# Kernel tuning notes

Hardware: AMD Instinct MI355X
Metric: run time of the kernel (lower is better)

The kernel has to match this reference:

```python
import jax, jax.numpy as jnp
import numpy as np

N, E = 100000, 1600000
DIN, DH, DOUT = 128, 64, 4


def setup_inputs() -> dict:
    key = jax.random.key(0)
    ks = jax.random.split(key, 16)
    dims = [(DIN, DH), (DH, DH), (DH, DH), (DH, DH), (DH, DH), (DH, DOUT)]
    inp = {
        "x": jax.random.normal(ks[0], (N, DIN), dtype=jnp.float32),
        "edge_index": jax.random.randint(ks[1], (2, E), 0, N, dtype=jnp.int32),
    }
    for i, (di, do) in enumerate(dims):
        scale = 1.0 / np.sqrt(di)
        inp[f"W{i}"] = jax.random.normal(ks[2 + i], (di, do), dtype=jnp.float32) * scale
        inp[f"b{i}"] = jnp.zeros((do,), dtype=jnp.float32)
    return inp


def _gcn_graph(edge_index, n):
    # PyG gcn_norm with self-loops: D^{-1/2} (A+I) D^{-1/2}
    loops = jnp.arange(n, dtype=edge_index.dtype)
    src = jnp.concatenate([edge_index[0], loops])  # message sources
    dst = jnp.concatenate([edge_index[1], loops])  # aggregation targets
    deg = jax.ops.segment_sum(jnp.ones(src.shape[0], jnp.float32), dst, num_segments=n)
    dinv = jnp.where(deg > 0, jax.lax.rsqrt(deg), 0.0)
    norm = dinv[src] * dinv[dst]  # [E+N]
    return src, dst, norm


def _gcn_layer(x, src, dst, norm, W, b, n):
    h = x @ W                                   # [N, dout] dense transform first (PyG order)
    msg = h[src] * norm[:, None]                # gather + scale, [E+N, dout]
    return jax.ops.segment_sum(msg, dst, num_segments=n) + b


def reference(x, edge_index, W0, b0, W1, b1, W2, b2, W3, b3, W4, b4, W5, b5):
    n = x.shape[0]
    src, dst, norm = _gcn_graph(edge_index, n)
    Ws = [W0, W1, W2, W3, W4, W5]
    bs = [b0, b1, b2, b3, b4, b5]
    for i in range(len(Ws)):
        x = _gcn_layer(x, src, dst, norm, Ws[i], bs[i], n)
        if i < len(Ws) - 1:
            # eval mode: dropout / edge_dropout are identity
            x = jnp.where(x >= 0, x, 0.2 * x)  # leaky_relu, negative_slope=0.2
    return x
```

## Files before the change

kernel.cpp:

```cpp
#include <hip/hip_runtime.h>


__device__ __forceinline__ float readlane_f(float v, int l) {
    union { float f; int i; } u;
    u.f = v;
    u.i = __builtin_amdgcn_readlane(u.i, l);
    return u.f;
}

__global__ __launch_bounds__(256) void bucket_hist(const int* __restrict__ dst,
                                                   int* __restrict__ ghist,
                                                   int E, int NB) {
    __shared__ int h[1024];
    for (int i = threadIdx.x; i < NB; i += 256) h[i] = 0;
    __syncthreads();
    int i = blockIdx.x * blockDim.x + threadIdx.x;
    int stride = gridDim.x * blockDim.x;
    for (; i < E; i += stride) atomicAdd(&h[dst[i] >> 7], 1);
    __syncthreads();
    for (int j = threadIdx.x; j < NB; j += 256) {
        int c = h[j];
        if (c) atomicAdd(&ghist[j], c);
    }
}

__global__ void bucket_scan(const int* __restrict__ ghist, int* __restrict__ base,
                            int* __restrict__ cursor, int NB, int E) {
    int tid = threadIdx.x, lane = tid & 63, wid = tid >> 6;
    int v = (tid < NB) ? ghist[tid] : 0;
    int incl = v;
#pragma unroll
    for (int off = 1; off < 64; off <<= 1) {
        int t = __shfl_up(incl, off);
        if (lane >= off) incl += t;
    }
    __shared__ int ws[16];
    if (lane == 63) ws[wid] = incl;
    __syncthreads();
    if (tid == 0) {
        int run = 0;
        for (int i = 0; i < 16; ++i) { int t = ws[i]; ws[i] = run; run += t; }
    }
    __syncthreads();
    int excl = ws[wid] + incl - v;
    if (tid < NB) { base[tid] = excl; cursor[tid] = excl; }
    if (tid == 0) base[NB] = E;
}

__global__ __launch_bounds__(256) void bucket_scatter(
    const int* __restrict__ src, const int* __restrict__ dst,
    int* __restrict__ cursor, int* __restrict__ bsrc,
    unsigned char* __restrict__ bdl, int E, int NB) {
    __shared__ int h[1024];
    __shared__ int rb[1024];
    const int CH = 4096;
    for (int c0 = blockIdx.x * CH; c0 < E; c0 += gridDim.x * CH) {
        int cend = c0 + CH < E ? c0 + CH : E;
        for (int j = threadIdx.x; j < NB; j += 256) h[j] = 0;
        __syncthreads();
        for (int i = c0 + threadIdx.x; i < cend; i += 256)
            atomicAdd(&h[dst[i] >> 7], 1);
        __syncthreads();
        for (int j = threadIdx.x; j < NB; j += 256) {
            int c = h[j];
            rb[j] = c ? atomicAdd(&cursor[j], c) : 0;
            h[j] = 0;
        }
        __syncthreads();
        for (int i = c0 + threadIdx.x; i < cend; i += 256) {
            int d = dst[i];
            int b = d >> 7;
            int p = rb[b] + atomicAdd(&h[b], 1);
            bsrc[p] = src[i];
            bdl[p] = (unsigned char)(d & 127);
        }
        __syncthreads();
    }
}

__global__ __launch_bounds__(256) void bucket_finalize(
    const int* __restrict__ base, const int* __restrict__ bsrc,
    const unsigned char* __restrict__ bdl, int* __restrict__ rowptr,
    int* __restrict__ ssrc, float* __restrict__ dinv, int N, int NB, int E) {
    __shared__ int cnt[128];
    __shared__ int cur[128];
    __shared__ int w0sum;
    const int tid = threadIdx.x;
    const int lane = tid & 63;
    for (int b = blockIdx.x; b < NB; b += gridDim.x) {
        const int s = base[b], e = base[b + 1];
        const int d0 = b << 7;
        const int w = (N - d0 < 128) ? (N - d0) : 128;
        if (tid < 128) cnt[tid] = 0;
        __syncthreads();
        for (int i = s + tid; i < e; i += 256) atomicAdd(&cnt[bdl[i]], 1);
        __syncthreads();
        int v = (tid < 128) ? cnt[tid] : 0;
        int incl = v;
#pragma unroll
        for (int off = 1; off < 64; off <<= 1) {
            int t = __shfl_up(incl, off);
            if (lane >= off) incl += t;
        }
        if (tid == 63) w0sum = incl;
        __syncthreads();
        int excl = incl - v + ((tid >= 64 && tid < 128) ? w0sum : 0);
        if (tid < 128) cur[tid] = s + excl;
        if (tid < w) {
            rowptr[d0 + tid] = s + excl;
            dinv[d0 + tid] = rsqrtf((float)(v + 1));
        }
        __syncthreads();
        for (int i = s + tid; i < e; i += 256) {
            int p = atomicAdd(&cur[bdl[i]], 1);
            ssrc[p] = bsrc[i];
        }
        __syncthreads();
    }
    if (blockIdx.x == 0 && tid == 0) rowptr[N] = E;
}

template <int K, bool LRELU>
__global__ __launch_bounds__(256) void gemm_hs(
    const float* __restrict__ in, const float* __restrict__ W,
    const float* __restrict__ dinv, float* __restrict__ hs, int n) {
    const int lane = threadIdx.x & 63;
    const int gw = blockIdx.x * (blockDim.x >> 6) + (threadIdx.x >> 6);
    const int nw = gridDim.x * (blockDim.x >> 6);

    float wreg[K];
#pragma unroll
    for (int k = 0; k < K; ++k) wreg[k] = W[k * 64 + lane];

    for (int row = gw; row < n; row += nw) {
        float xv0 = in[(size_t)row * K + lane];
        if (LRELU) xv0 = xv0 >= 0.f ? xv0 : 0.2f * xv0;
        float xv1 = 0.f;
        if (K == 128) xv1 = in[(size_t)row * K + 64 + lane];
        float a0 = 0.f, a1 = 0.f, a2 = 0.f, a3 = 0.f;
#pragma unroll
        for (int k = 0; k < 64; k += 4) {
            a0 = fmaf(readlane_f(xv0, k + 0), wreg[k + 0], a0);
            a1 = fmaf(readlane_f(xv0, k + 1), wreg[k + 1], a1);
            a2 = fmaf(readlane_f(xv0, k + 2), wreg[k + 2], a2);
            a3 = fmaf(readlane_f(xv0, k + 3), wreg[k + 3], a3);
        }
        if (K == 128) {
#pragma unroll
            for (int k = 0; k < 64; k += 4) {
                a0 = fmaf(readlane_f(xv1, k + 0), wreg[64 + k + 0], a0);
                a1 = fmaf(readlane_f(xv1, k + 1), wreg[64 + k + 1], a1);
                a2 = fmaf(readlane_f(xv1, k + 2), wreg[64 + k + 2], a2);
                a3 = fmaf(readlane_f(xv1, k + 3), wreg[64 + k + 3], a3);
            }
        }
        float acc = (a0 + a1) + (a2 + a3);
        hs[(size_t)row * 64 + lane] = dinv[row] * acc;
    }
}

__global__ __launch_bounds__(256) void csr_agg_stream(
    const float* __restrict__ hs, const int* __restrict__ rowptr,
    const int* __restrict__ ssrc, const float* __restrict__ dinv,
    const float* __restrict__ b, float* __restrict__ y,
    int N, int E, int nwaves) {
    const int lane = threadIdx.x & 63;
    const int w = blockIdx.x * (blockDim.x >> 6) + (threadIdx.x >> 6);
    if (w >= nwaves) return;
    const float bl = b[lane];

    auto lb = [&](long long t) {
        int lo = 0, hi = N;
        while (lo < hi) {
            int m = (lo + hi) >> 1;
            if ((long long)rowptr[m] < t) lo = m + 1; else hi = m;
        }
        return lo;
    };
    const long long q0 = (long long)w * E / nwaves;
    const long long q1 = (long long)(w + 1) * E / nwaves;
    int r0 = lb(q0);
    int r1 = (w == nwaves - 1) ? N : lb(q1);

    for (int d = r0; d < r1; ++d) {
        int e = __builtin_amdgcn_readfirstlane(rowptr[d]);
        const int end = __builtin_amdgcn_readfirstlane(rowptr[d + 1]);
        float acc0 = hs[(size_t)d * 64 + lane];
        float acc1 = 0.f;
        for (; e + 8 <= end; e += 8) {
            int s0 = ssrc[e + 0], s1 = ssrc[e + 1];
            int s2 = ssrc[e + 2], s3 = ssrc[e + 3];
            int s4 = ssrc[e + 4], s5 = ssrc[e + 5];
            int s6 = ssrc[e + 6], s7 = ssrc[e + 7];
            float v0 = hs[(size_t)s0 * 64 + lane];
            float v1 = hs[(size_t)s1 * 64 + lane];
            float v2 = hs[(size_t)s2 * 64 + lane];
            float v3 = hs[(size_t)s3 * 64 + lane];
            float v4 = hs[(size_t)s4 * 64 + lane];
            float v5 = hs[(size_t)s5 * 64 + lane];
            float v6 = hs[(size_t)s6 * 64 + lane];
            float v7 = hs[(size_t)s7 * 64 + lane];
            acc0 += v0 + v2;
            acc1 += v1 + v3;
            acc0 += v4 + v6;
            acc1 += v5 + v7;
        }
        for (; e < end; ++e) {
            int s = ssrc[e];
            acc0 += hs[(size_t)s * 64 + lane];
        }
        y[(size_t)d * 64 + lane] = fmaf(dinv[d], acc0 + acc1, bl);
    }
}

__global__ __launch_bounds__(256) void gemm4_hs(
    const float* __restrict__ y, const float* __restrict__ W,
    const float* __restrict__ dinv, float* __restrict__ hs4, int n) {
    int i = blockIdx.x * blockDim.x + threadIdx.x;
    int stride = gridDim.x * blockDim.x;
    for (; i < n; i += stride) {
        const float4* xr = (const float4*)(y + (size_t)i * 64);
        float a0 = 0.f, a1 = 0.f, a2 = 0.f, a3 = 0.f;
#pragma unroll
        for (int k4 = 0; k4 < 16; ++k4) {
            float4 xv = xr[k4];
            float e0 = xv.x >= 0.f ? xv.x : 0.2f * xv.x;
            float e1 = xv.y >= 0.f ? xv.y : 0.2f * xv.y;
            float e2 = xv.z >= 0.f ? xv.z : 0.2f * xv.z;
            float e3 = xv.w >= 0.f ? xv.w : 0.2f * xv.w;
            int k = k4 * 4;
            a0 = fmaf(e0, W[(k + 0) * 4 + 0], a0); a1 = fmaf(e0, W[(k + 0) * 4 + 1], a1);
            a2 = fmaf(e0, W[(k + 0) * 4 + 2], a2); a3 = fmaf(e0, W[(k + 0) * 4 + 3], a3);
            a0 = fmaf(e1, W[(k + 1) * 4 + 0], a0); a1 = fmaf(e1, W[(k + 1) * 4 + 1], a1);
            a2 = fmaf(e1, W[(k + 1) * 4 + 2], a2); a3 = fmaf(e1, W[(k + 1) * 4 + 3], a3);
            a0 = fmaf(e2, W[(k + 2) * 4 + 0], a0); a1 = fmaf(e2, W[(k + 2) * 4 + 1], a1);
            a2 = fmaf(e2, W[(k + 2) * 4 + 2], a2); a3 = fmaf(e2, W[(k + 2) * 4 + 3], a3);
            a0 = fmaf(e3, W[(k + 3) * 4 + 0], a0); a1 = fmaf(e3, W[(k + 3) * 4 + 1], a1);
            a2 = fmaf(e3, W[(k + 3) * 4 + 2], a2); a3 = fmaf(e3, W[(k + 3) * 4 + 3], a3);
        }
        float di = dinv[i];
        ((float4*)hs4)[i] = make_float4(di * a0, di * a1, di * a2, di * a3);
    }
}

__global__ __launch_bounds__(256) void csr_agg4(
    const float* __restrict__ hs4, const int* __restrict__ rowptr,
    const int* __restrict__ ssrc, const float* __restrict__ dinv,
    const float* __restrict__ b, float* __restrict__ out, int n) {
    int i = blockIdx.x * blockDim.x + threadIdx.x;
    int stride = gridDim.x * blockDim.x;
    float b0 = b[0], b1 = b[1], b2 = b[2], b3 = b[3];
    for (; i < n; i += stride) {
        float4 hv = ((const float4*)hs4)[i];
        float a0 = hv.x, a1 = hv.y, a2 = hv.z, a3 = hv.w;
        int e = rowptr[i], end = rowptr[i + 1];
        for (; e < end; ++e) {
            int s = ssrc[e];
            float4 v = ((const float4*)hs4)[s];
            a0 += v.x; a1 += v.y; a2 += v.z; a3 += v.w;
        }
        float di = dinv[i];
        ((float4*)out)[i] = make_float4(fmaf(di, a0, b0), fmaf(di, a1, b1),
                                        fmaf(di, a2, b2), fmaf(di, a3, b3));
    }
}

static inline size_t al64(size_t x) { return (x + 63) & ~(size_t)63; }

extern "C" void kernel_launch(void* const* d_in, const int* in_sizes, int n_in,
                              void* d_out, int out_size, void* d_ws, size_t ws_size,
                              hipStream_t stream) {
    const float* x  = (const float*)d_in[0];
    const int* ei   = (const int*)d_in[1];
    const float* W0 = (const float*)d_in[2];
    const float* b0 = (const float*)d_in[3];
    const float* W1 = (const float*)d_in[4];
    const float* b1 = (const float*)d_in[5];
    const float* W2 = (const float*)d_in[6];
    const float* b2 = (const float*)d_in[7];
    const float* W3 = (const float*)d_in[8];
    const float* b3 = (const float*)d_in[9];
    const float* W4 = (const float*)d_in[10];
    const float* b4 = (const float*)d_in[11];
    const float* W5 = (const float*)d_in[12];
    const float* b5 = (const float*)d_in[13];

    const int N = in_sizes[0] / 128;
    const int E = in_sizes[1] / 2;
    const int* src  = ei;
    const int* dstp = ei + E;
    const int NB = (N + 127) >> 7;

    float* ws = (float*)d_ws;
    size_t off = 0;
    int*   rowptr = (int*)(ws + off);   off += al64((size_t)N + 1);
    float* dinv   = ws + off;           off += al64((size_t)N);
    int*   ssrc   = (int*)(ws + off);   off += al64((size_t)E);
    float* bufA   = ws + off;           off += (size_t)64 * N;
    float* bufB   = ws + off;

    int* ghist = (int*)bufA;
    int* bbase = ghist + 1024;
    int* bcur  = bbase + 1088;
    int* bsrc  = (int*)(bufA + 4096);
    unsigned char* bdl = (unsigned char*)(bsrc + E);

    hipMemsetAsync(ghist, 0, 1024 * sizeof(int), stream);
    bucket_hist<<<391, 256, 0, stream>>>(dstp, ghist, E, NB);
    bucket_scan<<<1, 1024, 0, stream>>>(ghist, bbase, bcur, NB, E);
    bucket_scatter<<<391, 256, 0, stream>>>(src, dstp, bcur, bsrc, bdl, E, NB);
    bucket_finalize<<<NB, 256, 0, stream>>>(bbase, bsrc, bdl, rowptr, ssrc, dinv, N, NB, E);

    const int AGG_BLOCKS = 2048;
    const int NWAVES = AGG_BLOCKS * 4;

    gemm_hs<128, false><<<2048, 256, 0, stream>>>(x, W0, dinv, bufA, N);
    csr_agg_stream<<<AGG_BLOCKS, 256, 0, stream>>>(bufA, rowptr, ssrc, dinv, b0, bufB, N, E, NWAVES);

    const float* Ws[4] = {W1, W2, W3, W4};
    const float* bs[4] = {b1, b2, b3, b4};
    for (int l = 0; l < 4; ++l) {
        gemm_hs<64, true><<<2048, 256, 0, stream>>>(bufB, Ws[l], dinv, bufA, N);
        csr_agg_stream<<<AGG_BLOCKS, 256, 0, stream>>>(bufA, rowptr, ssrc, dinv, bs[l], bufB, N, E, NWAVES);
    }

    gemm4_hs<<<1024, 256, 0, stream>>>(bufB, W5, dinv, bufA, N);
    csr_agg4<<<512, 256, 0, stream>>>(bufA, rowptr, ssrc, dinv, b5, (float*)d_out, N);
}
```

Baseline: 613.7 us.

## Fuse aggregation with next layer's dense transform and leaky-relu

Each CSR aggregation kernel now applies bias, leaky-relu and the next layer's weight multiply in-register, using readlane broadcasts (wave shuffle-reduction for the 4-wide output), and writes the next layer's scaled features directly. This removes the separate GEMM kernels and their full write and re-read of the 100k×64 intermediate each layer, and drops five launches. Index loads become nontemporal to avoid polluting cache. The cost is 64 extra weight registers per aggregation thread, which may lower occupancy for a latency-bound gather.

```diff
diff --git a/kernel.cpp b/kernel.cpp
--- a/kernel.cpp
+++ b/kernel.cpp
@@ -120,23 +120,20 @@
     if (blockIdx.x == 0 && tid == 0) rowptr[N] = E;
 }
 
-template <int K, bool LRELU>
-__global__ __launch_bounds__(256) void gemm_hs(
+__global__ __launch_bounds__(256) void gemm0_hs(
     const float* __restrict__ in, const float* __restrict__ W,
     const float* __restrict__ dinv, float* __restrict__ hs, int n) {
     const int lane = threadIdx.x & 63;
     const int gw = blockIdx.x * (blockDim.x >> 6) + (threadIdx.x >> 6);
     const int nw = gridDim.x * (blockDim.x >> 6);
 
-    float wreg[K];
-#pragma unroll
-    for (int k = 0; k < K; ++k) wreg[k] = W[k * 64 + lane];
+    float wreg[128];
+#pragma unroll
+    for (int k = 0; k < 128; ++k) wreg[k] = W[k * 64 + lane];
 
     for (int row = gw; row < n; row += nw) {
-        float xv0 = in[(size_t)row * K + lane];
-        if (LRELU) xv0 = xv0 >= 0.f ? xv0 : 0.2f * xv0;
-        float xv1 = 0.f;
-        if (K == 128) xv1 = in[(size_t)row * K + 64 + lane];
+        float xv0 = in[(size_t)row * 128 + lane];
+        float xv1 = in[(size_t)row * 128 + 64 + lane];
         float a0 = 0.f, a1 = 0.f, a2 = 0.f, a3 = 0.f;
 #pragma unroll
         for (int k = 0; k < 64; k += 4) {
@@ -145,29 +142,31 @@
             a2 = fmaf(readlane_f(xv0, k + 2), wreg[k + 2], a2);
             a3 = fmaf(readlane_f(xv0, k + 3), wreg[k + 3], a3);
         }
-        if (K == 128) {
-#pragma unroll
-            for (int k = 0; k < 64; k += 4) {
-                a0 = fmaf(readlane_f(xv1, k + 0), wreg[64 + k + 0], a0);
-                a1 = fmaf(readlane_f(xv1, k + 1), wreg[64 + k + 1], a1);
-                a2 = fmaf(readlane_f(xv1, k + 2), wreg[64 + k + 2], a2);
-                a3 = fmaf(readlane_f(xv1, k + 3), wreg[64 + k + 3], a3);
-            }
+#pragma unroll
+        for (int k = 0; k < 64; k += 4) {
+            a0 = fmaf(readlane_f(xv1, k + 0), wreg[64 + k + 0], a0);
+            a1 = fmaf(readlane_f(xv1, k + 1), wreg[64 + k + 1], a1);
+            a2 = fmaf(readlane_f(xv1, k + 2), wreg[64 + k + 2], a2);
+            a3 = fmaf(readlane_f(xv1, k + 3), wreg[64 + k + 3], a3);
         }
         float acc = (a0 + a1) + (a2 + a3);
         hs[(size_t)row * 64 + lane] = dinv[row] * acc;
     }
 }
 
-__global__ __launch_bounds__(256) void csr_agg_stream(
+__global__ __launch_bounds__(256) void agg_gemm64(
     const float* __restrict__ hs, const int* __restrict__ rowptr,
     const int* __restrict__ ssrc, const float* __restrict__ dinv,
-    const float* __restrict__ b, float* __restrict__ y,
-    int N, int E, int nwaves) {
+    const float* __restrict__ b, const float* __restrict__ W,
+    float* __restrict__ hs_next, int N, int E, int nwaves) {
     const int lane = threadIdx.x & 63;
     const int w = blockIdx.x * (blockDim.x >> 6) + (threadIdx.x >> 6);
     if (w >= nwaves) return;
     const float bl = b[lane];
+
+    float wreg[64];
+#pragma unroll
+    for (int k = 0; k < 64; ++k) wreg[k] = W[k * 64 + lane];
 
     auto lb = [&](long long t) {
         int lo = 0, hi = N;
@@ -188,10 +187,14 @@
         float acc0 = hs[(size_t)d * 64 + lane];
         float acc1 = 0.f;
         for (; e + 8 <= end; e += 8) {
-            int s0 = ssrc[e + 0], s1 = ssrc[e + 1];
-            int s2 = ssrc[e + 2], s3 = ssrc[e + 3];
-            int s4 = ssrc[e + 4], s5 = ssrc[e + 5];
-            int s6 = ssrc[e + 6], s7 = ssrc[e + 7];
+            int s0 = __builtin_nontemporal_load(ssrc + e + 0);
+            int s1 = __builtin_nontemporal_load(ssrc + e + 1);
+            int s2 = __builtin_nontemporal_load(ssrc + e + 2);
+            int s3 = __builtin_nontemporal_load(ssrc + e + 3);
+            int s4 = __builtin_nontemporal_load(ssrc + e + 4);
+            int s5 = __builtin_nontemporal_load(ssrc + e + 5);
+            int s6 = __builtin_nontemporal_load(ssrc + e + 6);
+            int s7 = __builtin_nontemporal_load(ssrc + e + 7);
             float v0 = hs[(size_t)s0 * 64 + lane];
             float v1 = hs[(size_t)s1 * 64 + lane];
             float v2 = hs[(size_t)s2 * 64 + lane];
@@ -206,40 +209,93 @@
             acc1 += v5 + v7;
         }
         for (; e < end; ++e) {
-            int s = ssrc[e];
+            int s = __builtin_nontemporal_load(ssrc + e);
             acc0 += hs[(size_t)s * 64 + lane];
         }
-        y[(size_t)d * 64 + lane] = fmaf(dinv[d], acc0 + acc1, bl);
-    }
-}
-
-__global__ __launch_bounds__(256) void gemm4_hs(
-    const float* __restrict__ y, const float* __restrict__ W,
-    const float* __restrict__ dinv, float* __restrict__ hs4, int n) {
-    int i = blockIdx.x * blockDim.x + threadIdx.x;
-    int stride = gridDim.x * blockDim.x;
-    for (; i < n; i += stride) {
-        const float4* xr = (const float4*)(y + (size_t)i * 64);
+        const float di = dinv[d];
+        float y = fmaf(di, acc0 + acc1, bl);
+        float xv = y >= 0.f ? y : 0.2f * y;
         float a0 = 0.f, a1 = 0.f, a2 = 0.f, a3 = 0.f;
 #pragma unroll
-        for (int k4 = 0; k4 < 16; ++k4) {
-            float4 xv = xr[k4];
-            float e0 = xv.x >= 0.f ? xv.x : 0.2f * xv.x;
-            float e1 = xv.y >= 0.f ? xv.y : 0.2f * xv.y;
-            float e2 = xv.z >= 0.f ? xv.z : 0.2f * xv.z;
-            float e3 = xv.w >= 0.f ? xv.w : 0.2f * xv.w;
-            int k = k4 * 4;
-            a0 = fmaf(e0, W[(k + 0) * 4 + 0], a0); a1 = fmaf(e0, W[(k + 0) * 4 + 1], a1);
-            a2 = fmaf(e0, W[(k + 0) * 4 + 2], a2); a3 = fmaf(e0, W[(k + 0) * 4 + 3], a3);
-            a0 = fmaf(e1, W[(k + 1) * 4 + 0], a0); a1 = fmaf(e1, W[(k + 1) * 4 + 1], a1);
-            a2 = fmaf(e1, W[(k + 1) * 4 + 2], a2); a3 = fmaf(e1, W[(k + 1) * 4 + 3], a3);
-            a0 = fmaf(e2, W[(k + 2) * 4 + 0], a0); a1 = fmaf(e2, W[(k + 2) * 4 + 1], a1);
-            a2 = fmaf(e2, W[(k + 2) * 4 + 2], a2); a3 = fmaf(e2, W[(k + 2) * 4 + 3], a3);
-            a0 = fmaf(e3, W[(k + 3) * 4 + 0], a0); a1 = fmaf(e3, W[(k + 3) * 4 + 1], a1);
-            a2 = fmaf(e3, W[(k + 3) * 4 + 2], a2); a3 = fmaf(e3, W[(k + 3) * 4 + 3], a3);
-        }
-        float di = dinv[i];
-        ((float4*)hs4)[i] = make_float4(di * a0, di * a1, di * a2, di * a3);
+        for (int k = 0; k < 64; k += 4) {
+            a0 = fmaf(readlane_f(xv, k + 0), wreg[k + 0], a0);
+            a1 = fmaf(readlane_f(xv, k + 1), wreg[k + 1], a1);
+            a2 = fmaf(readlane_f(xv, k + 2), wreg[k + 2], a2);
+            a3 = fmaf(readlane_f(xv, k + 3), wreg[k + 3], a3);
+        }
+        float h = (a0 + a1) + (a2 + a3);
+        hs_next[(size_t)d * 64 + lane] = di * h;
+    }
+}
+
+__global__ __launch_bounds__(256) void agg_gemm4(
+    const float* __restrict__ hs, const int* __restrict__ rowptr,
+    const int* __restrict__ ssrc, const float* __restrict__ dinv,
+    const float* __restrict__ b, const float* __restrict__ W,
+    float* __restrict__ hs4, int N, int E, int nwaves) {
+    const int lane = threadIdx.x & 63;
+    const int w = blockIdx.x * (blockDim.x >> 6) + (threadIdx.x >> 6);
+    if (w >= nwaves) return;
+    const float bl = b[lane];
+    const float4 w4 = *(const float4*)(W + lane * 4);
+
+    auto lb = [&](long long t) {
+        int lo = 0, hi = N;
+        while (lo < hi) {
+            int m = (lo + hi) >> 1;
+            if ((long long)rowptr[m] < t) lo = m + 1; else hi = m;
+        }
+        return lo;
+    };
+    const long long q0 = (long long)w * E / nwaves;
+    const long long q1 = (long long)(w + 1) * E / nwaves;
+    int r0 = lb(q0);
+    int r1 = (w == nwaves - 1) ? N : lb(q1);
+
+    for (int d = r0; d < r1; ++d) {
+        int e = __builtin_amdgcn_readfirstlane(rowptr[d]);
+        const int end = __builtin_amdgcn_readfirstlane(rowptr[d + 1]);
+        float acc0 = hs[(size_t)d * 64 + lane];
+        float acc1 = 0.f;
+        for (; e + 8 <= end; e += 8) {
+            int s0 = __builtin_nontemporal_load(ssrc + e + 0);
+            int s1 = __builtin_nontemporal_load(ssrc + e + 1);
+            int s2 = __builtin_nontemporal_load(ssrc + e + 2);
+            int s3 = __builtin_nontemporal_load(ssrc + e + 3);
+            int s4 = __builtin_nontemporal_load(ssrc + e + 4);
+            int s5 = __builtin_nontemporal_load(ssrc + e + 5);
+            int s6 = __builtin_nontemporal_load(ssrc + e + 6);
+            int s7 = __builtin_nontemporal_load(ssrc + e + 7);
+            float v0 = hs[(size_t)s0 * 64 + lane];
+            float v1 = hs[(size_t)s1 * 64 + lane];
+            float v2 = hs[(size_t)s2 * 64 + lane];
+            float v3 = hs[(size_t)s3 * 64 + lane];
+            float v4 = hs[(size_t)s4 * 64 + lane];
+            float v5 = hs[(size_t)s5 * 64 + lane];
+            float v6 = hs[(size_t)s6 * 64 + lane];
+            float v7 = hs[(size_t)s7 * 64 + lane];
+            acc0 += v0 + v2;
+            acc1 += v1 + v3;
+            acc0 += v4 + v6;
+            acc1 += v5 + v7;
+        }
+        for (; e < end; ++e) {
+            int s = __builtin_nontemporal_load(ssrc + e);
+            acc0 += hs[(size_t)s * 64 + lane];
+        }
+        const float di = dinv[d];
+        float y = fmaf(di, acc0 + acc1, bl);
+        float xv = y >= 0.f ? y : 0.2f * y;
+        float p0 = xv * w4.x, p1 = xv * w4.y, p2 = xv * w4.z, p3 = xv * w4.w;
+#pragma unroll
+        for (int off = 1; off < 64; off <<= 1) {
+            p0 += __shfl_xor(p0, off);
+            p1 += __shfl_xor(p1, off);
+            p2 += __shfl_xor(p2, off);
+            p3 += __shfl_xor(p3, off);
+        }
+        if (lane == 0)
+            ((float4*)hs4)[d] = make_float4(di * p0, di * p1, di * p2, di * p3);
     }
 }
 
@@ -314,16 +370,14 @@
     const int AGG_BLOCKS = 2048;
     const int NWAVES = AGG_BLOCKS * 4;
 
-    gemm_hs<128, false><<<2048, 256, 0, stream>>>(x, W0, dinv, bufA, N);
-    csr_agg_stream<<<AGG_BLOCKS, 256, 0, stream>>>(bufA, rowptr, ssrc, dinv, b0, bufB, N, E, NWAVES);
-
-    const float* Ws[4] = {W1, W2, W3, W4};
-    const float* bs[4] = {b1, b2, b3, b4};
-    for (int l = 0; l < 4; ++l) {
-        gemm_hs<64, true><<<2048, 256, 0, stream>>>(bufB, Ws[l], dinv, bufA, N);
-        csr_agg_stream<<<AGG_BLOCKS, 256, 0, stream>>>(bufA, rowptr, ssrc, dinv, bs[l], bufB, N, E, NWAVES);
-    }
-
-    gemm4_hs<<<1024, 256, 0, stream>>>(bufB, W5, dinv, bufA, N);
-    csr_agg4<<<512, 256, 0, stream>>>(bufA, rowptr, ssrc, dinv, b5, (float*)d_out, N);
-}
+    gemm0_hs<<<2048, 256, 0, stream>>>(x, W0, dinv, bufA, N);
+
+    agg_gemm64<<<AGG_BLOCKS, 256, 0, stream>>>(bufA, rowptr, ssrc, dinv, b0, W1, bufB, N, E, NWAVES);
+    agg_gemm64<<<AGG_BLOCKS, 256, 0, stream>>>(bufB, rowptr, ssrc, dinv, b1, W2, bufA, N, E, NWAVES);
+    agg_gemm64<<<AGG_BLOCKS, 256, 0, stream>>>(bufA, rowptr, ssrc, dinv, b2, W3, bufB, N, E, NWAVES);
+    agg_gemm64<<<AGG_BLOCKS, 256, 0, stream>>>(bufB, rowptr, ssrc, dinv, b3, W4, bufA, N, E, NWAVES);
+
+    agg_gemm4<<<AGG_BLOCKS, 256, 0, stream>>>(bufA, rowptr, ssrc, dinv, b4, W5, bufB, N, E, NWAVES);
+
+    csr_agg4<<<1024, 256, 0, stream>>>(bufB, rowptr, ssrc, dinv, b5, (float*)d_out, N);
+}
```

Measured after the change: 639.5 us. 1.04x slower.

## Split feature halves across blocks in CSR aggregation and fuse leaky-ReLU into aggregation

Applied to the files above, without the earlier changes.

Rewrites the 64-wide CSR aggregation so each wave handles 32 features of a row, with its two half-waves processing alternate edges and combining results via a cross-lane shuffle. Blocks are interleaved so each feature half is spread across the grid, probably to improve cache locality of the gathers. The leaky-ReLU moves from the GEMM input into the aggregation epilogue, and edge indices use nontemporal loads. Rows are now assigned by simple strided looping instead of edge-balanced binary-search partitioning, and the final aggregation grid is doubled. Each row's index list is now read twice, once per feature half, and load balancing may be worse for high-degree rows.

```diff
diff --git a/kernel.cpp b/kernel.cpp
--- a/kernel.cpp
+++ b/kernel.cpp
@@ -120,7 +120,7 @@
     if (blockIdx.x == 0 && tid == 0) rowptr[N] = E;
 }
 
-template <int K, bool LRELU>
+template <int K>
 __global__ __launch_bounds__(256) void gemm_hs(
     const float* __restrict__ in, const float* __restrict__ W,
     const float* __restrict__ dinv, float* __restrict__ hs, int n) {
@@ -134,7 +134,6 @@
 
     for (int row = gw; row < n; row += nw) {
         float xv0 = in[(size_t)row * K + lane];
-        if (LRELU) xv0 = xv0 >= 0.f ? xv0 : 0.2f * xv0;
         float xv1 = 0.f;
         if (K == 128) xv1 = in[(size_t)row * K + 64 + lane];
         float a0 = 0.f, a1 = 0.f, a2 = 0.f, a3 = 0.f;
@@ -159,84 +158,73 @@
     }
 }
 
-__global__ __launch_bounds__(256) void csr_agg_stream(
+__global__ __launch_bounds__(256) void csr_agg_half(
     const float* __restrict__ hs, const int* __restrict__ rowptr,
     const int* __restrict__ ssrc, const float* __restrict__ dinv,
-    const float* __restrict__ b, float* __restrict__ y,
-    int N, int E, int nwaves) {
+    const float* __restrict__ b, float* __restrict__ xact, int N) {
     const int lane = threadIdx.x & 63;
-    const int w = blockIdx.x * (blockDim.x >> 6) + (threadIdx.x >> 6);
-    if (w >= nwaves) return;
-    const float bl = b[lane];
-
-    auto lb = [&](long long t) {
-        int lo = 0, hi = N;
-        while (lo < hi) {
-            int m = (lo + hi) >> 1;
-            if ((long long)rowptr[m] < t) lo = m + 1; else hi = m;
-        }
-        return lo;
-    };
-    const long long q0 = (long long)w * E / nwaves;
-    const long long q1 = (long long)(w + 1) * E / nwaves;
-    int r0 = lb(q0);
-    int r1 = (w == nwaves - 1) ? N : lb(q1);
-
-    for (int d = r0; d < r1; ++d) {
+    const int wid = threadIdx.x >> 6;
+    const int sl = (blockIdx.x & 7) >> 2;
+    const int sb = (blockIdx.x >> 3) * 4 + (blockIdx.x & 3);
+    const int w = sb * 4 + wid;
+    const int nw = (gridDim.x >> 1) * 4;
+    const int g = lane >> 5;
+    const int f = lane & 31;
+    const int off = sl * 32 + f;
+    const float bl = b[off];
+
+    for (int d = w; d < N; d += nw) {
         int e = __builtin_amdgcn_readfirstlane(rowptr[d]);
         const int end = __builtin_amdgcn_readfirstlane(rowptr[d + 1]);
-        float acc0 = hs[(size_t)d * 64 + lane];
+        float acc0 = (g == 0) ? hs[(size_t)d * 64 + off] : 0.f;
         float acc1 = 0.f;
         for (; e + 8 <= end; e += 8) {
-            int s0 = ssrc[e + 0], s1 = ssrc[e + 1];
-            int s2 = ssrc[e + 2], s3 = ssrc[e + 3];
-            int s4 = ssrc[e + 4], s5 = ssrc[e + 5];
-            int s6 = ssrc[e + 6], s7 = ssrc[e + 7];
-            float v0 = hs[(size_t)s0 * 64 + lane];
-            float v1 = hs[(size_t)s1 * 64 + lane];
-            float v2 = hs[(size_t)s2 * 64 + lane];
-            float v3 = hs[(size_t)s3 * 64 + lane];
-            float v4 = hs[(size_t)s4 * 64 + lane];
-            float v5 = hs[(size_t)s5 * 64 + lane];
-            float v6 = hs[(size_t)s6 * 64 + lane];
-            float v7 = hs[(size_t)s7 * 64 + lane];
+            int s0 = __builtin_nontemporal_load(ssrc + e + 0 + g);
+            int s1 = __builtin_nontemporal_load(ssrc + e + 2 + g);
+            int s2 = __builtin_nontemporal_load(ssrc + e + 4 + g);
+            int s3 = __builtin_nontemporal_load(ssrc + e + 6 + g);
+            float v0 = hs[(size_t)s0 * 64 + off];
+            float v1 = hs[(size_t)s1 * 64 + off];
+            float v2 = hs[(size_t)s2 * 64 + off];
+            float v3 = hs[(size_t)s3 * 64 + off];
             acc0 += v0 + v2;
             acc1 += v1 + v3;
-            acc0 += v4 + v6;
-            acc1 += v5 + v7;
-        }
-        for (; e < end; ++e) {
-            int s = ssrc[e];
-            acc0 += hs[(size_t)s * 64 + lane];
-        }
-        y[(size_t)d * 64 + lane] = fmaf(dinv[d], acc0 + acc1, bl);
+        }
+        for (; e < end; e += 2) {
+            int idx = e + g;
+            if (idx < end) {
+                int s = __builtin_nontemporal_load(ssrc + idx);
+                acc0 += hs[(size_t)s * 64 + off];
+            }
+        }
+        float acc = acc0 + acc1;
+        acc += __shfl_xor(acc, 32);
+        float y = fmaf(dinv[d], acc, bl);
+        y = y >= 0.f ? y : 0.2f * y;
+        if (g == 0) xact[(size_t)d * 64 + off] = y;
     }
 }
 
 __global__ __launch_bounds__(256) void gemm4_hs(
-    const float* __restrict__ y, const float* __restrict__ W,
+    const float* __restrict__ xact, const float* __restrict__ W,
     const float* __restrict__ dinv, float* __restrict__ hs4, int n) {
     int i = blockIdx.x * blockDim.x + threadIdx.x;
     int stride = gridDim.x * blockDim.x;
     for (; i < n; i += stride) {
-        const float4* xr = (const float4*)(y + (size_t)i * 64);
+        const float4* xr = (const float4*)(xact + (size_t)i * 64);
         float a0 = 0.f, a1 = 0.f, a2 = 0.f, a3 = 0.f;
 #pragma unroll
         for (int k4 = 0; k4 < 16; ++k4) {
             float4 xv = xr[k4];
-            float e0 = xv.x >= 0.f ? xv.x : 0.2f * xv.x;
-            float e1 = xv.y >= 0.f ? xv.y : 0.2f * xv.y;
-            float e2 = xv.z >= 0.f ? xv.z : 0.2f * xv.z;
-            float e3 = xv.w >= 0.f ? xv.w : 0.2f * xv.w;
             int k = k4 * 4;
-            a0 = fmaf(e0, W[(k + 0) * 4 + 0], a0); a1 = fmaf(e0, W[(k + 0) * 4 + 1], a1);
-            a2 = fmaf(e0, W[(k + 0) * 4 + 2], a2); a3 = fmaf(e0, W[(k + 0) * 4 + 3], a3);
-            a0 = fmaf(e1, W[(k + 1) * 4 + 0], a0); a1 = fmaf(e1, W[(k + 1) * 4 + 1], a1);
-            a2 = fmaf(e1, W[(k + 1) * 4 + 2], a2); a3 = fmaf(e1, W[(k + 1) * 4 + 3], a3);
-            a0 = fmaf(e2, W[(k + 2) * 4 + 0], a0); a1 = fmaf(e2, W[(k + 2) * 4 + 1], a1);
-            a2 = fmaf(e2, W[(k + 2) * 4 + 2], a2); a3 = fmaf(e2, W[(k + 2) * 4 + 3], a3);
-            a0 = fmaf(e3, W[(k + 3) * 4 + 0], a0); a1 = fmaf(e3, W[(k + 3) * 4 + 1], a1);
-            a2 = fmaf(e3, W[(k + 3) * 4 + 2], a2); a3 = fmaf(e3, W[(k + 3) * 4 + 3], a3);
+            a0 = fmaf(xv.x, W[(k + 0) * 4 + 0], a0); a1 = fmaf(xv.x, W[(k + 0) * 4 + 1], a1);
+            a2 = fmaf(xv.x, W[(k + 0) * 4 + 2], a2); a3 = fmaf(xv.x, W[(k + 0) * 4 + 3], a3);
+            a0 = fmaf(xv.y, W[(k + 1) * 4 + 0], a0); a1 = fmaf(xv.y, W[(k + 1) * 4 + 1], a1);
+            a2 = fmaf(xv.y, W[(k + 1) * 4 + 2], a2); a3 = fmaf(xv.y, W[(k + 1) * 4 + 3], a3);
+            a0 = fmaf(xv.z, W[(k + 2) * 4 + 0], a0); a1 = fmaf(xv.z, W[(k + 2) * 4 + 1], a1);
+            a2 = fmaf(xv.z, W[(k + 2) * 4 + 2], a2); a3 = fmaf(xv.z, W[(k + 2) * 4 + 3], a3);
+            a0 = fmaf(xv.w, W[(k + 3) * 4 + 0], a0); a1 = fmaf(xv.w, W[(k + 3) * 4 + 1], a1);
+            a2 = fmaf(xv.w, W[(k + 3) * 4 + 2], a2); a3 = fmaf(xv.w, W[(k + 3) * 4 + 3], a3);
         }
         float di = dinv[i];
         ((float4*)hs4)[i] = make_float4(di * a0, di * a1, di * a2, di * a3);
@@ -312,18 +300,17 @@
     bucket_finalize<<<NB, 256, 0, stream>>>(bbase, bsrc, bdl, rowptr, ssrc, dinv, N, NB, E);
 
     const int AGG_BLOCKS = 2048;
-    const int NWAVES = AGG_BLOCKS * 4;
-
-    gemm_hs<128, false><<<2048, 256, 0, stream>>>(x, W0, dinv, bufA, N);
-    csr_agg_stream<<<AGG_BLOCKS, 256, 0, stream>>>(bufA, rowptr, ssrc, dinv, b0, bufB, N, E, NWAVES);
+
+    gemm_hs<128><<<2048, 256, 0, stream>>>(x, W0, dinv, bufA, N);
+    csr_agg_half<<<AGG_BLOCKS, 256, 0, stream>>>(bufA, rowptr, ssrc, dinv, b0, bufB, N);
 
     const float* Ws[4] = {W1, W2, W3, W4};
     const float* bs[4] = {b1, b2, b3, b4};
     for (int l = 0; l < 4; ++l) {
-        gemm_hs<64, true><<<2048, 256, 0, stream>>>(bufB, Ws[l], dinv, bufA, N);
-        csr_agg_stream<<<AGG_BLOCKS, 256, 0, stream>>>(bufA, rowptr, ssrc, dinv, bs[l], bufB, N, E, NWAVES);
+        gemm_hs<64><<<2048, 256, 0, stream>>>(bufB, Ws[l], dinv, bufA, N);
+        csr_agg_half<<<AGG_BLOCKS, 256, 0, stream>>>(bufA, rowptr, ssrc, dinv, bs[l], bufB, N);
     }
 
     gemm4_hs<<<1024, 256, 0, stream>>>(bufB, W5, dinv, bufA, N);
-    csr_agg4<<<512, 256, 0, stream>>>(bufA, rowptr, ssrc, dinv, b5, (float*)d_out, N);
-}
+    csr_agg4<<<1024, 256, 0, stream>>>(bufA, rowptr, ssrc, dinv, b5, (float*)d_out, N);
+}
```

Measured after the change: 797.1 us. 1.3x slower.
